# Kernel optimization log

Measured on AMD Instinct MI355X. Metric: run time of the kernel, lower is better.

## Reference

```python
import jax, jax.numpy as jnp
import numpy as np
import math

D_MODEL = 1024
N_HEADS = 16
B, S = 4, 2048

def _xavier(key, shape):
    fan_out, fan_in = shape
    limit = math.sqrt(6.0 / (fan_in + fan_out))
    return jax.random.uniform(key, shape, jnp.float32, -limit, limit)

def setup_inputs() -> dict:
    key = jax.random.key(0)
    kx, kqkv, ko = jax.random.split(key, 3)
    x = jax.random.normal(kx, (B, S, D_MODEL), dtype=jnp.float32)
    W_qkv = _xavier(kqkv, (3 * D_MODEL, D_MODEL))
    W_o = _xavier(ko, (D_MODEL, D_MODEL))
    return {"x": x, "W_qkv": W_qkv, "W_o": W_o}

def reference(x, W_qkv, W_o):
    Bx, Sx, D = x.shape
    H = N_HEADS
    d_h = D // H
    T = jnp.einsum('bsd,ed->bse', x, W_qkv)          # (B,S,3D)
    Q, K, V = jnp.split(T, 3, axis=-1)
    # (B,S,D) -> (B,H,S,d_h)
    Q = Q.reshape(Bx, Sx, H, d_h).transpose(0, 2, 1, 3)
    K = K.reshape(Bx, Sx, H, d_h).transpose(0, 2, 1, 3)
    V = V.reshape(Bx, Sx, H, d_h).transpose(0, 2, 1, 3)
    scores = jnp.einsum('bhqd,bhkd->bhqk', Q, K) / jnp.sqrt(jnp.float32(d_h))
    attn = jax.nn.softmax(scores, axis=-1)
    out = jnp.einsum('bhqk,bhkd->bhqd', attn, V)
    out = out.transpose(0, 2, 1, 3).reshape(Bx, Sx, D)
    Y = jnp.einsum('bsd,ed->bse', out, W_o)
    return Y
```

## Files before the change

kernel.cpp:

```cpp
#include <hip/hip_runtime.h>
#include <stdint.h>

#define SS 2048

typedef __attribute__((ext_vector_type(8))) short short8;
typedef __attribute__((ext_vector_type(4))) float f32x4;
typedef __attribute__((ext_vector_type(16))) float f32x16;

static __device__ __forceinline__ unsigned short f2bf(float f) {
    uint32_t u = __builtin_bit_cast(uint32_t, f);
    u += 0x7fffu + ((u >> 16) & 1u);
    return (unsigned short)(u >> 16);
}

static __device__ __forceinline__ uint32_t cvtpk(float lo, float hi) {
    uint32_t r;
    asm("v_cvt_pk_bf16_f32 %0, %1, %2" : "=v"(r) : "v"(lo), "v"(hi));
    return r;
}

static __device__ __forceinline__ void async16(const unsigned short* g, unsigned short* l) {
    __builtin_amdgcn_global_load_lds(
        (const __attribute__((address_space(1))) uint32_t*)g,
        (__attribute__((address_space(3))) uint32_t*)l, 16, 0, 0);
}

__global__ void cast3(const float* __restrict__ a, const float* __restrict__ b,
                      const float* __restrict__ c,
                      unsigned short* __restrict__ da, unsigned short* __restrict__ db,
                      unsigned short* __restrict__ dc_) {
    int i = (blockIdx.x * 256 + threadIdx.x) * 4;
    const float* s;
    unsigned short* d;
    if (i < 8388608)        { s = a + i;              d = da + i; }
    else if (i < 11534336)  { s = b + (i - 8388608);  d = db + (i - 8388608); }
    else                    { s = c + (i - 11534336); d = dc_ + (i - 11534336); }
    float4 v = *(const float4*)s;
    ushort4 o;
    o.x = f2bf(v.x); o.y = f2bf(v.y); o.z = f2bf(v.z); o.w = f2bf(v.w);
    *(ushort4*)d = o;
}

template<int MODE>
__global__ void gemm_bt(const unsigned short* __restrict__ A,
                        const unsigned short* __restrict__ Bm,
                        void* __restrict__ Cout,
                        unsigned short* __restrict__ Vt,
                        int K) {
    __shared__ unsigned short As[128 * 64];
    __shared__ unsigned short Bs[128 * 64];
    const int t = threadIdx.x;
    const int w = t >> 6, l = t & 63;
    const int wm = w >> 1, wn = w & 1;
    const int l15 = l & 15, l4 = l >> 4;
    const int m0 = blockIdx.x * 128, n0 = blockIdx.y * 128;
    const int srow = t >> 3;
    const int scol = (t & 7) * 8;

    f32x4 acc[4][4] = {};

    for (int k0 = 0; k0 < K; k0 += 64) {
#pragma unroll
        for (int r = 0; r < 4; ++r) {
            int row = r * 32 + srow;
            async16(A + (size_t)(m0 + row) * K + k0 + scol, (unsigned short*)&As[row * 64 + scol]);
        }
#pragma unroll
        for (int r = 0; r < 4; ++r) {
            int row = r * 32 + srow;
            async16(Bm + (size_t)(n0 + row) * K + k0 + scol, (unsigned short*)&Bs[row * 64 + scol]);
        }
        __syncthreads();
#pragma unroll
        for (int kk = 0; kk < 64; kk += 32) {
            short8 af[4], bfr[4];
#pragma unroll
            for (int m = 0; m < 4; ++m)
                af[m] = *(const short8*)&As[(wm * 64 + m * 16 + l15) * 64 + kk + l4 * 8];
#pragma unroll
            for (int n = 0; n < 4; ++n)
                bfr[n] = *(const short8*)&Bs[(wn * 64 + n * 16 + l15) * 64 + kk + l4 * 8];
#pragma unroll
            for (int m = 0; m < 4; ++m)
#pragma unroll
                for (int n = 0; n < 4; ++n)
                    acc[m][n] = __builtin_amdgcn_mfma_f32_16x16x32_bf16(af[m], bfr[n], acc[m][n], 0, 0, 0);
        }
        __syncthreads();
    }

#pragma unroll
    for (int m = 0; m < 4; ++m) {
        int rbase = m0 + wm * 64 + m * 16 + l4 * 4;
#pragma unroll
        for (int n = 0; n < 4; ++n) {
            int c = n0 + wn * 64 + n * 16 + l15;
            f32x4 v = acc[m][n];
            if (MODE == 0) {
                if (c < 2048) {
                    float sc = (c < 1024) ? 0.18033688f : 1.0f;
                    unsigned short* T = (unsigned short*)Cout;
#pragma unroll
                    for (int r = 0; r < 4; ++r)
                        T[(size_t)(rbase + r) * 2048 + c] = f2bf(v[0 + r] * sc);
                } else {
                    int vv = c - 2048;
                    int hh = vv >> 6, d = vv & 63;
                    int bb = rbase >> 11, s = rbase & 2047;
                    ushort4 pk;
                    pk.x = f2bf(v[0]); pk.y = f2bf(v[1]); pk.z = f2bf(v[2]); pk.w = f2bf(v[3]);
                    *(ushort4*)&Vt[((size_t)(bb * 16 + hh) * 64 + d) * 2048 + s] = pk;
                }
            } else {
                float* C = (float*)Cout;
#pragma unroll
                for (int r = 0; r < 4; ++r)
                    C[(size_t)(rbase + r) * 1024 + c] = v[r];
            }
        }
    }
}

__global__ __launch_bounds__(256, 4) void attn_kernel(
        const unsigned short* __restrict__ Tqk,
        const unsigned short* __restrict__ Vt,
        unsigned short* __restrict__ Out) {
    __shared__ unsigned short Ks[2][64 * 64];
    __shared__ unsigned short Vs[2][64 * 64];
    const int t = threadIdx.x;
    const int w = t >> 6, l = t & 63;
    const int lq = l & 31, hfl = l >> 5;

    const int lin = blockIdx.x;
    const int j = lin >> 3;
    const int bh = (lin & 7) * 8 + (j & 7);
    const int qt = j >> 3;
    const int b = bh >> 4, hh = bh & 15;
    const int qrow = qt * 128 + w * 32 + lq;

    short8 qf[4];
    const size_t trow = ((size_t)b * SS + qrow) * 2048;
#pragma unroll
    for (int dc = 0; dc < 4; ++dc)
        qf[dc] = *(const short8*)&Tqk[trow + hh * 64 + dc * 16 + hfl * 8];

    char* KsB = (char*)Ks;
    char* VsB = (char*)Vs;

    const int swcol = ((l & 7) ^ (l >> 3)) * 8;
    const unsigned short* kga = Tqk + (size_t)b * SS * 2048 + 1024 + hh * 64
                              + (size_t)(w * 16 + (l >> 3)) * 2048 + swcol;
    const unsigned short* kgb = kga + 8 * 2048;
    const unsigned short* vga = Vt + (size_t)bh * 64 * 2048
                              + (size_t)(w * 16 + (l >> 3)) * 2048 + swcol;
    const unsigned short* vgb = vga + 8 * 2048;
    const int ldw = w * 16 * 128;

#define STAGE(buf)                                                                   \
    {                                                                                \
        char* kd = KsB + (buf) * 8192 + ldw;                                         \
        char* vd = VsB + (buf) * 8192 + ldw;                                         \
        async16(kga, (unsigned short*)kd);                                           \
        async16(kgb, (unsigned short*)(kd + 1024));                                  \
        async16(vga, (unsigned short*)vd);                                           \
        async16(vgb, (unsigned short*)(vd + 1024));                                  \
    }

    f32x16 oacc[2] = {};
    f32x16 lacc = {};
    short8 ones;
#pragma unroll
    for (int i = 0; i < 8; ++i) ones[i] = (short)0x3F80;

    STAGE(0);
    asm volatile("s_waitcnt vmcnt(0)" ::: "memory");
    __syncthreads();

    for (int it = 0; it < 32; ++it) {
        const int cur = it & 1;
        const char* kb = KsB + cur * 8192;
        const char* vb = VsB + cur * 8192;
        if (it < 31) {
            kga += 64 * 2048; kgb += 64 * 2048;
            vga += 64;        vgb += 64;
            STAGE(cur ^ 1);
        }

        f32x16 sa[2] = {};
        __builtin_amdgcn_s_setprio(1);
#pragma unroll
        for (int kvt = 0; kvt < 2; ++kvt) {
            int row = kvt * 32 + lq;
#pragma unroll
            for (int dc = 0; dc < 4; ++dc) {
                short8 kf = *(const short8*)(kb + row * 128 + ((dc * 32 + hfl * 16) ^ ((row & 7) << 4)));
                sa[kvt] = __builtin_amdgcn_mfma_f32_32x32x16_bf16(kf, qf[dc], sa[kvt], 0, 0, 0);
            }
        }
        __builtin_amdgcn_s_setprio(0);

#pragma unroll
        for (int kvt = 0; kvt < 2; ++kvt)
#pragma unroll
            for (int r = 0; r < 16; ++r)
                sa[kvt][r] = __builtin_amdgcn_exp2f(sa[kvt][r]);

        short8 pb[4];
#pragma unroll
        for (int c = 0; c < 4; ++c) {
            int f = c >> 1, r0 = (c & 1) * 8;
            uint32_t v0 = cvtpk(sa[f][r0 + 0], sa[f][r0 + 1]);
            uint32_t v1 = cvtpk(sa[f][r0 + 2], sa[f][r0 + 3]);
            uint32_t v2 = cvtpk(sa[f][r0 + 4], sa[f][r0 + 5]);
            uint32_t v3 = cvtpk(sa[f][r0 + 6], sa[f][r0 + 7]);
            asm("v_permlane32_swap_b32 %0, %1" : "+v"(v0), "+v"(v2));
            asm("v_permlane32_swap_b32 %0, %1" : "+v"(v1), "+v"(v3));
            union { uint32_t u[4]; short8 s; } pbu;
            pbu.u[0] = v0;
            pbu.u[1] = v1;
            pbu.u[2] = v2;
            pbu.u[3] = v3;
            pb[c] = pbu.s;
        }

        __builtin_amdgcn_s_setprio(1);
#pragma unroll
        for (int dt = 0; dt < 2; ++dt) {
            int row0 = dt * 32 + lq;
#pragma unroll
            for (int c = 0; c < 4; ++c) {
                short8 vf = *(const short8*)(vb + row0 * 128 + ((c * 32 + hfl * 16) ^ ((row0 & 7) << 4)));
                oacc[dt] = __builtin_amdgcn_mfma_f32_32x32x16_bf16(vf, pb[c], oacc[dt], 0, 0, 0);
            }
        }
#pragma unroll
        for (int c = 0; c < 4; ++c)
            lacc = __builtin_amdgcn_mfma_f32_32x32x16_bf16(ones, pb[c], lacc, 0, 0, 0);
        __builtin_amdgcn_s_setprio(0);

        asm volatile("s_waitcnt vmcnt(0)" ::: "memory");
        __syncthreads();
    }
#undef STAGE

    float inv = 1.0f / lacc[0];
    const size_t obase = ((size_t)b * SS + qrow) * 1024 + hh * 64;
#pragma unroll
    for (int dt = 0; dt < 2; ++dt)
#pragma unroll
        for (int r = 0; r < 16; ++r) {
            int d = dt * 32 + (r & 3) + 8 * (r >> 2) + 4 * hfl;
            Out[obase + d] = f2bf(oacc[dt][r] * inv);
        }
}

extern "C" void kernel_launch(void* const* d_in, const int* in_sizes, int n_in,
                              void* d_out, int out_size, void* d_ws, size_t ws_size,
                              hipStream_t stream) {
    const float* x    = (const float*)d_in[0];
    const float* wqkv = (const float*)d_in[1];
    const float* wo   = (const float*)d_in[2];

    unsigned short* ws  = (unsigned short*)d_ws;
    unsigned short* xb  = ws;
    unsigned short* w1  = ws + 8388608;
    unsigned short* w2  = ws + 11534336;
    unsigned short* vt  = ws + 12582912;
    unsigned short* ao  = ws + 20971520;
    unsigned short* tqk = (unsigned short*)d_out;

    cast3<<<12288, 256, 0, stream>>>(x, wqkv, wo, xb, w1, w2);
    gemm_bt<0><<<dim3(64, 24), 256, 0, stream>>>(xb, w1, (void*)tqk, vt, 1024);
    attn_kernel<<<1024, 256, 0, stream>>>(tqk, vt, ao);
    gemm_bt<1><<<dim3(64, 8), 256, 0, stream>>>(ao, w2, d_out, nullptr, 1024);
}
```

Before: 192.0 us.

## Process two KV tiles per iteration with four-deep LDS buffering in attention

The attention loop now handles two 64-key tiles per iteration across four LDS buffers. Both QK matmuls are issued before the exp/PV stages, and the next pair of tiles is prefetched while the current pair is computed. This halves the number of barriers and vmcnt waits and gives more independent MFMA work between syncs. In exchange, LDS use doubles to 64KB and launch bounds drop to 2 blocks per CU, which lowers occupancy.

```diff
diff --git a/kernel.cpp b/kernel.cpp
--- a/kernel.cpp
+++ b/kernel.cpp
@@ -121,12 +121,12 @@
     }
 }
 
-__global__ __launch_bounds__(256, 4) void attn_kernel(
+__global__ __launch_bounds__(256, 2) void attn_kernel(
         const unsigned short* __restrict__ Tqk,
         const unsigned short* __restrict__ Vt,
         unsigned short* __restrict__ Out) {
-    __shared__ unsigned short Ks[2][64 * 64];
-    __shared__ unsigned short Vs[2][64 * 64];
+    __shared__ unsigned short Ks[4][64 * 64];
+    __shared__ unsigned short Vs[4][64 * 64];
     const int t = threadIdx.x;
     const int w = t >> 6, l = t & 63;
     const int lq = l & 31, hfl = l >> 5;
@@ -148,23 +148,66 @@
     char* VsB = (char*)Vs;
 
     const int swcol = ((l & 7) ^ (l >> 3)) * 8;
-    const unsigned short* kga = Tqk + (size_t)b * SS * 2048 + 1024 + hh * 64
-                              + (size_t)(w * 16 + (l >> 3)) * 2048 + swcol;
-    const unsigned short* kgb = kga + 8 * 2048;
-    const unsigned short* vga = Vt + (size_t)bh * 64 * 2048
-                              + (size_t)(w * 16 + (l >> 3)) * 2048 + swcol;
-    const unsigned short* vgb = vga + 8 * 2048;
+    const unsigned short* kg = Tqk + (size_t)b * SS * 2048 + 1024 + hh * 64
+                             + (size_t)(w * 16 + (l >> 3)) * 2048 + swcol;
+    const unsigned short* vg = Vt + (size_t)bh * 64 * 2048
+                             + (size_t)(w * 16 + (l >> 3)) * 2048 + swcol;
     const int ldw = w * 16 * 128;
 
-#define STAGE(buf)                                                                   \
+#define STAGE(bf, tt)                                                                \
     {                                                                                \
-        char* kd = KsB + (buf) * 8192 + ldw;                                         \
-        char* vd = VsB + (buf) * 8192 + ldw;                                         \
-        async16(kga, (unsigned short*)kd);                                           \
-        async16(kgb, (unsigned short*)(kd + 1024));                                  \
-        async16(vga, (unsigned short*)vd);                                           \
-        async16(vgb, (unsigned short*)(vd + 1024));                                  \
-    }
+        char* kd = KsB + (bf) * 8192 + ldw;                                          \
+        char* vd = VsB + (bf) * 8192 + ldw;                                          \
+        const unsigned short* kp = kg + (size_t)(tt) * (64 * 2048);                  \
+        const unsigned short* vp = vg + (tt) * 64;                                   \
+        async16(kp, (unsigned short*)kd);                                            \
+        async16(kp + 8 * 2048, (unsigned short*)(kd + 1024));                        \
+        async16(vp, (unsigned short*)vd);                                            \
+        async16(vp + 8 * 2048, (unsigned short*)(vd + 1024));                        \
+    }
+
+#define QK(sa, kb)                                                                   \
+    __builtin_amdgcn_s_setprio(1);                                                   \
+    _Pragma("unroll") for (int kvt = 0; kvt < 2; ++kvt) {                            \
+        int row = kvt * 32 + lq;                                                     \
+        _Pragma("unroll") for (int dc = 0; dc < 4; ++dc) {                           \
+            short8 kf = *(const short8*)((kb) + row * 128 +                          \
+                ((dc * 32 + hfl * 16) ^ ((row & 7) << 4)));                          \
+            sa[kvt] = __builtin_amdgcn_mfma_f32_32x32x16_bf16(kf, qf[dc], sa[kvt], 0, 0, 0); \
+        }                                                                            \
+    }                                                                                \
+    __builtin_amdgcn_s_setprio(0);
+
+#define EXPPACK(sa, pb)                                                              \
+    _Pragma("unroll") for (int kvt = 0; kvt < 2; ++kvt)                              \
+        _Pragma("unroll") for (int r = 0; r < 16; ++r)                               \
+            sa[kvt][r] = __builtin_amdgcn_exp2f(sa[kvt][r]);                         \
+    _Pragma("unroll") for (int c = 0; c < 4; ++c) {                                  \
+        int f = c >> 1, r0 = (c & 1) * 8;                                            \
+        uint32_t v0 = cvtpk(sa[f][r0 + 0], sa[f][r0 + 1]);                           \
+        uint32_t v1 = cvtpk(sa[f][r0 + 2], sa[f][r0 + 3]);                           \
+        uint32_t v2 = cvtpk(sa[f][r0 + 4], sa[f][r0 + 5]);                           \
+        uint32_t v3 = cvtpk(sa[f][r0 + 6], sa[f][r0 + 7]);                           \
+        asm("v_permlane32_swap_b32 %0, %1" : "+v"(v0), "+v"(v2));                    \
+        asm("v_permlane32_swap_b32 %0, %1" : "+v"(v1), "+v"(v3));                    \
+        union { uint32_t u[4]; short8 s; } pbu;                                      \
+        pbu.u[0] = v0; pbu.u[1] = v1; pbu.u[2] = v2; pbu.u[3] = v3;                  \
+        pb[c] = pbu.s;                                                               \
+    }
+
+#define PV(pb, vb)                                                                   \
+    __builtin_amdgcn_s_setprio(1);                                                   \
+    _Pragma("unroll") for (int dt = 0; dt < 2; ++dt) {                               \
+        int row0 = dt * 32 + lq;                                                     \
+        _Pragma("unroll") for (int c = 0; c < 4; ++c) {                              \
+            short8 vf = *(const short8*)((vb) + row0 * 128 +                         \
+                ((c * 32 + hfl * 16) ^ ((row0 & 7) << 4)));                          \
+            oacc[dt] = __builtin_amdgcn_mfma_f32_32x32x16_bf16(vf, pb[c], oacc[dt], 0, 0, 0); \
+        }                                                                            \
+    }                                                                                \
+    _Pragma("unroll") for (int c = 0; c < 4; ++c)                                    \
+        lacc = __builtin_amdgcn_mfma_f32_32x32x16_bf16(ones, pb[c], lacc, 0, 0, 0);  \
+    __builtin_amdgcn_s_setprio(0);
 
     f32x16 oacc[2] = {};
     f32x16 lacc = {};
@@ -172,76 +215,41 @@
 #pragma unroll
     for (int i = 0; i < 8; ++i) ones[i] = (short)0x3F80;
 
-    STAGE(0);
+    STAGE(0, 0);
+    STAGE(1, 1);
     asm volatile("s_waitcnt vmcnt(0)" ::: "memory");
     __syncthreads();
 
-    for (int it = 0; it < 32; ++it) {
-        const int cur = it & 1;
-        const char* kb = KsB + cur * 8192;
-        const char* vb = VsB + cur * 8192;
-        if (it < 31) {
-            kga += 64 * 2048; kgb += 64 * 2048;
-            vga += 64;        vgb += 64;
-            STAGE(cur ^ 1);
-        }
-
-        f32x16 sa[2] = {};
-        __builtin_amdgcn_s_setprio(1);
-#pragma unroll
-        for (int kvt = 0; kvt < 2; ++kvt) {
-            int row = kvt * 32 + lq;
-#pragma unroll
-            for (int dc = 0; dc < 4; ++dc) {
-                short8 kf = *(const short8*)(kb + row * 128 + ((dc * 32 + hfl * 16) ^ ((row & 7) << 4)));
-                sa[kvt] = __builtin_amdgcn_mfma_f32_32x32x16_bf16(kf, qf[dc], sa[kvt], 0, 0, 0);
-            }
-        }
-        __builtin_amdgcn_s_setprio(0);
-
-#pragma unroll
-        for (int kvt = 0; kvt < 2; ++kvt)
-#pragma unroll
-            for (int r = 0; r < 16; ++r)
-                sa[kvt][r] = __builtin_amdgcn_exp2f(sa[kvt][r]);
-
+    for (int i = 0; i < 16; ++i) {
+        const int ba = (i & 1) << 1;
+        const int bb = ba | 1;
+        const char* kbA = KsB + ba * 8192;
+        const char* vbA = VsB + ba * 8192;
+        const char* kbB = KsB + bb * 8192;
+        const char* vbB = VsB + bb * 8192;
+        const bool more = (i < 15);
+
+        f32x16 saA[2] = {}, saB[2] = {};
         short8 pb[4];
-#pragma unroll
-        for (int c = 0; c < 4; ++c) {
-            int f = c >> 1, r0 = (c & 1) * 8;
-            uint32_t v0 = cvtpk(sa[f][r0 + 0], sa[f][r0 + 1]);
-            uint32_t v1 = cvtpk(sa[f][r0 + 2], sa[f][r0 + 3]);
-            uint32_t v2 = cvtpk(sa[f][r0 + 4], sa[f][r0 + 5]);
-            uint32_t v3 = cvtpk(sa[f][r0 + 6], sa[f][r0 + 7]);
-            asm("v_permlane32_swap_b32 %0, %1" : "+v"(v0), "+v"(v2));
-            asm("v_permlane32_swap_b32 %0, %1" : "+v"(v1), "+v"(v3));
-            union { uint32_t u[4]; short8 s; } pbu;
-            pbu.u[0] = v0;
-            pbu.u[1] = v1;
-            pbu.u[2] = v2;
-            pbu.u[3] = v3;
-            pb[c] = pbu.s;
-        }
-
-        __builtin_amdgcn_s_setprio(1);
-#pragma unroll
-        for (int dt = 0; dt < 2; ++dt) {
-            int row0 = dt * 32 + lq;
-#pragma unroll
-            for (int c = 0; c < 4; ++c) {
-                short8 vf = *(const short8*)(vb + row0 * 128 + ((c * 32 + hfl * 16) ^ ((row0 & 7) << 4)));
-                oacc[dt] = __builtin_amdgcn_mfma_f32_32x32x16_bf16(vf, pb[c], oacc[dt], 0, 0, 0);
-            }
-        }
-#pragma unroll
-        for (int c = 0; c < 4; ++c)
-            lacc = __builtin_amdgcn_mfma_f32_32x32x16_bf16(ones, pb[c], lacc, 0, 0, 0);
-        __builtin_amdgcn_s_setprio(0);
+
+        if (more) STAGE(ba ^ 2, 2 * i + 2);
+        QK(saA, kbA);
+        if (more) STAGE(bb ^ 2, 2 * i + 3);
+        QK(saB, kbB);
+
+        EXPPACK(saA, pb);
+        PV(pb, vbA);
+
+        EXPPACK(saB, pb);
+        PV(pb, vbB);
 
         asm volatile("s_waitcnt vmcnt(0)" ::: "memory");
         __syncthreads();
     }
 #undef STAGE
+#undef QK
+#undef EXPPACK
+#undef PV
 
     float inv = 1.0f / lacc[0];
     const size_t obase = ((size_t)b * SS + qrow) * 1024 + hh * 64;
```

Result: slower. 199.1 us (+3.7%).
